# Kernel optimization log

Hardware: AMD Instinct MI355X
Metric: run time of the kernel (lower is better)

## Reference

```python
import jax, jax.numpy as jnp
import numpy as np

IN, MID, OUT = 512, 512, 512
B, S = 8, 1024
SLOPE = 0.01  # torch leaky_relu default


def _linear_params(key, fan_in, fan_out):
    # torch nn.Linear default init: U(-1/sqrt(fan_in), 1/sqrt(fan_in)) per real/imag part
    ks = jax.random.split(key, 4)
    bound = 1.0 / np.sqrt(fan_in)
    wr = jax.random.uniform(ks[0], (fan_out, fan_in), jnp.float32, -bound, bound)
    wi = jax.random.uniform(ks[1], (fan_out, fan_in), jnp.float32, -bound, bound)
    br = jax.random.uniform(ks[2], (fan_out,), jnp.float32, -bound, bound)
    bi = jax.random.uniform(ks[3], (fan_out,), jnp.float32, -bound, bound)
    return wr, wi, br, bi


def setup_inputs() -> dict:
    key = jax.random.key(0)
    ks = jax.random.split(key, 7)
    inp = {
        'x_real': jax.random.normal(ks[0], (B, S, IN), jnp.float32),
        'x_imag': jax.random.normal(ks[1], (B, S, IN), jnp.float32),
    }
    for name, k, fi, fo in [('l1', ks[2], IN, MID), ('q', ks[3], MID, MID),
                            ('k', ks[4], MID, MID), ('v', ks[5], MID, MID),
                            ('l2', ks[6], MID, OUT)]:
        wr, wi, br, bi = _linear_params(k, fi, fo)
        inp[f'{name}_wr'], inp[f'{name}_wi'] = wr, wi
        inp[f'{name}_br'], inp[f'{name}_bi'] = br, bi
    return inp


def _clin(x, wr, wi, br, bi):
    w = (wr + 1j * wi).astype(jnp.complex64)
    b = (br + 1j * bi).astype(jnp.complex64)
    return x @ w.T + b


def _lrelu_c(z):
    r = jnp.where(z.real >= 0, z.real, SLOPE * z.real)
    i = jnp.where(z.imag >= 0, z.imag, SLOPE * z.imag)
    return r + 1j * i


def reference(x_real, x_imag,
              l1_wr, l1_wi, l1_br, l1_bi,
              q_wr, q_wi, q_br, q_bi,
              k_wr, k_wi, k_br, k_bi,
              v_wr, v_wi, v_br, v_bi,
              l2_wr, l2_wi, l2_br, l2_bi):
    x = (x_real + 1j * x_imag).astype(jnp.complex64)
    y = _lrelu_c(_clin(x, l1_wr, l1_wi, l1_br, l1_bi))
    q = _clin(y, q_wr, q_wi, q_br, q_bi)
    k = _clin(y, k_wr, k_wi, k_br, k_bi)
    v = _clin(y, v_wr, v_wi, v_br, v_bi)
    scores = jnp.einsum('bsd,btd->bst', q, k) / jnp.sqrt(jnp.float32(MID))
    attn = jax.nn.softmax(jnp.abs(scores), axis=-1).astype(jnp.complex64)
    weighted = jnp.einsum('bst,btd->bsd', attn, v)
    out = _clin(weighted, l2_wr, l2_wi, l2_br, l2_bi)
    # return real/imag stacked as float32 for harness comparability
    return jnp.stack([out.real, out.imag], axis=0)
```

## Files before the change

### kernel.cpp

```cpp
#include <hip/hip_runtime.h>
#include <hip/hip_bf16.h>
#include <stdint.h>

typedef __hip_bfloat16 bf16;
typedef __attribute__((ext_vector_type(8))) short short8;
typedef __attribute__((ext_vector_type(4))) float f32x4;

#define DEVI __device__ __forceinline__

static constexpr long IMAG_OFF = 8192l * 512;

DEVI unsigned short f2b(float f) {
  bf16 h = __float2bfloat16(f);
  unsigned short u;
  __builtin_memcpy(&u, &h, 2);
  return u;
}

#define GLD16(g, l) __builtin_amdgcn_global_load_lds( \
    (const __attribute__((address_space(1))) void*)(g), \
    (__attribute__((address_space(3))) void*)(l), 16, 0, 0)

__global__ __launch_bounds__(256) void pack_x_kernel(
    const float* __restrict__ xr, const float* __restrict__ xi,
    unsigned short* __restrict__ xp) {
  const int t = blockIdx.x * 256 + threadIdx.x;
  const int m = t >> 8;
  const int d = (t & 255) * 4;
  const float* src = (d < 512) ? (xr + (long)m * 512 + d)
                               : (xi + (long)m * 512 + (d - 512));
  float4 v = *reinterpret_cast<const float4*>(src);
  ushort4 o;
  o.x = f2b(v.x); o.y = f2b(v.y); o.z = f2b(v.z); o.w = f2b(v.w);
  *reinterpret_cast<ushort4*>(xp + (long)m * 1024 + d) = o;
}

struct WArgs {
  const float* wr[5]; const float* wi[5];
  const float* br[5]; const float* bi[5];
};

__global__ __launch_bounds__(256) void pack_w_kernel(
    WArgs a, unsigned short* __restrict__ W, float* __restrict__ bias) {
  const int L = blockIdx.z;
  const int t = blockIdx.x * 256 + threadIdx.x;
  const int n = t >> 8;
  const int k = (t & 255) * 4;
  const float* wr = a.wr[L]; const float* wi = a.wi[L];
  const float* src; float sgn = 1.0f;
  if (n < 512) {
    if (k < 512) src = wr + (long)n * 512 + k;
    else { src = wi + (long)n * 512 + (k - 512); sgn = -1.0f; }
  } else {
    if (k < 512) src = wi + (long)(n - 512) * 512 + k;
    else         src = wr + (long)(n - 512) * 512 + (k - 512);
  }
  float4 v = *reinterpret_cast<const float4*>(src);
  ushort4 o;
  o.x = f2b(sgn * v.x); o.y = f2b(sgn * v.y);
  o.z = f2b(sgn * v.z); o.w = f2b(sgn * v.w);
  *reinterpret_cast<ushort4*>(W + (long)L * 1024 * 1024 + (long)n * 1024 + k) = o;
  if (t < 1024)
    bias[L * 1024 + t] = (t < 512) ? a.br[L][t] : a.bi[L][t - 512];
}

template<int OM, bool BIAS, bool ACT>
__global__ __launch_bounds__(512) void gemm3_kernel(
    const bf16* __restrict__ A, const bf16* __restrict__ Bm,
    void* __restrict__ C0, void* __restrict__ C1, void* __restrict__ C2,
    const float* __restrict__ bias, int N, int K, long sA, long sB, long sC) {
  __shared__ __align__(16) bf16 sm[3 * 12288];
  const int tid  = threadIdx.x;
  const int lane = tid & 63, wave = tid >> 6;
  const int r = lane & 15, g = lane >> 4;
  const int wr = wave >> 2, wc = wave & 3;
  const int m0 = blockIdx.x * 128, n0 = blockIdx.y * 256;
  const int z  = blockIdx.z;

  const bf16* Ab = A  + (long)z * sA;
  const bf16* Bb = Bm + (long)z * sB;
  const int srow = tid >> 2;
  const int schk = ((tid & 3) ^ ((tid >> 3) & 3)) * 8;
  const bf16* gA  = Ab + (long)(m0 + srow) * K + schk;
  const bf16* gB0 = Bb + (long)(n0 + srow) * K + schk;
  const bf16* gB1 = gB0 + (long)128 * K;
  char* const lb = (char*)sm + tid * 16;

#define STG3(buf, kt) do { \
    GLD16(gA  + (kt), lb + (buf) * 24576); \
    GLD16(gB0 + (kt), lb + (buf) * 24576 + 8192); \
    GLD16(gB1 + (kt), lb + (buf) * 24576 + 16384); } while (0)

  f32x4 acc[4][4] = {};
  const int sel = (g ^ ((r >> 1) & 3)) * 8;
  const int axoff = (wr * 64 + r) * 32 + sel;
  const int bxoff = 4096 + (wc * 64 + r) * 32 + sel;

  STG3(0, 0);
  STG3(1, 32);
  asm volatile("s_waitcnt vmcnt(3)" ::: "memory");
  __builtin_amdgcn_s_barrier();

  const int nt = K >> 5;
  int bc = 0, bs = 2;
  for (int t = 0; t < nt; ++t) {
    if (t + 2 < nt) STG3(bs, (t + 2) << 5);
    const bf16* S = sm + bc * 12288;
    short8 af[4], bq[4];
#pragma unroll
    for (int mi = 0; mi < 4; ++mi)
      af[mi] = *reinterpret_cast<const short8*>(S + axoff + mi * 512);
#pragma unroll
    for (int nj = 0; nj < 4; ++nj)
      bq[nj] = *reinterpret_cast<const short8*>(S + bxoff + nj * 512);
    __builtin_amdgcn_s_setprio(1);
#pragma unroll
    for (int mi = 0; mi < 4; ++mi)
#pragma unroll
      for (int nj = 0; nj < 4; ++nj)
        acc[mi][nj] = __builtin_amdgcn_mfma_f32_16x16x32_bf16(bq[nj], af[mi], acc[mi][nj], 0, 0, 0);
    __builtin_amdgcn_s_setprio(0);
    if (t < nt - 2) asm volatile("s_waitcnt vmcnt(3)" ::: "memory");
    else            asm volatile("s_waitcnt vmcnt(0)" ::: "memory");
    __builtin_amdgcn_s_barrier();
    bc = (bc == 2) ? 0 : bc + 1;
    bs = (bs == 2) ? 0 : bs + 1;
  }
#undef STG3

  const int rowbase = m0 + wr * 64 + r;
  const int colbase = n0 + wc * 64 + g * 4;
#pragma unroll
  for (int mi = 0; mi < 4; ++mi) {
    const long rm = rowbase + mi * 16;
#pragma unroll
    for (int nj = 0; nj < 4; ++nj) {
      const int cn = colbase + nj * 16;
      float4 f;
      f.x = acc[mi][nj][0]; f.y = acc[mi][nj][1];
      f.z = acc[mi][nj][2]; f.w = acc[mi][nj][3];
      if (BIAS) {
        float4 b4 = *reinterpret_cast<const float4*>(bias + cn);
        f.x += b4.x; f.y += b4.y; f.z += b4.z; f.w += b4.w;
      }
      if (ACT) {
        f.x = (f.x >= 0.f) ? f.x : 0.01f * f.x;
        f.y = (f.y >= 0.f) ? f.y : 0.01f * f.y;
        f.z = (f.z >= 0.f) ? f.z : 0.01f * f.z;
        f.w = (f.w >= 0.f) ? f.w : 0.01f * f.w;
      }
      if (OM == 0) {
        unsigned short* C = (unsigned short*)C0 + (long)z * sC;
        ushort4 o; o.x = f2b(f.x); o.y = f2b(f.y); o.z = f2b(f.z); o.w = f2b(f.w);
        *reinterpret_cast<ushort4*>(C + rm * N + cn) = o;
      } else if (OM == 2) {
        float* O = (float*)C0;
        if (cn < 512) *reinterpret_cast<float4*>(O + rm * 512 + cn) = f;
        else          *reinterpret_cast<float4*>(O + IMAG_OFF + rm * 512 + (cn - 512)) = f;
      } else if (OM == 3) {
        float* S = (float*)C0 + (long)z * sC;
        const float scale = 0.044194173824159216f;
        float2 mg;
        mg.x = sqrtf(f.x * f.x + f.y * f.y) * scale;
        mg.y = sqrtf(f.z * f.z + f.w * f.w) * scale;
        *reinterpret_cast<float2*>(S + rm * 1024 + (cn >> 1)) = mg;
      } else if (OM == 4) {
        if (cn < 1024) {
          unsigned short* Q = (unsigned short*)C0;
          ushort4 o; o.x = f2b(f.x); o.y = f2b(f.y); o.z = f2b(f.z); o.w = f2b(f.w);
          *reinterpret_cast<ushort4*>(Q + rm * 1024 + cn) = o;
        } else if (cn < 2048) {
          const int d = cn - 1024;
          const int b = (int)(rm >> 10), tt = (int)(rm & 1023);
          unsigned short* KM = (unsigned short*)C1;
          const float s = (d < 512) ? 1.0f : -1.0f;
          ushort4 o1, o2;
          o1.x = f2b(s * f.x); o1.y = f2b(s * f.y);
          o1.z = f2b(s * f.z); o1.w = f2b(s * f.w);
          o2.x = f2b(f.x); o2.y = f2b(f.y); o2.z = f2b(f.z); o2.w = f2b(f.w);
          *reinterpret_cast<ushort4*>(KM + ((long)(b << 11) + 2 * tt)     * 1024 + d)         = o1;
          *reinterpret_cast<ushort4*>(KM + ((long)(b << 11) + 2 * tt + 1) * 1024 + (d ^ 512)) = o2;
        } else {
          unsigned short* V = (unsigned short*)C2;
          ushort4 o; o.x = f2b(f.x); o.y = f2b(f.y); o.z = f2b(f.z); o.w = f2b(f.w);
          *reinterpret_cast<ushort4*>(V + rm * 1024 + (cn - 2048)) = o;
        }
      }
    }
  }
}

DEVI float wred_max(float v) {
#pragma unroll
  for (int o = 32; o > 0; o >>= 1) v = fmaxf(v, __shfl_xor(v, o));
  return v;
}
DEVI float wred_sum(float v) {
#pragma unroll
  for (int o = 32; o > 0; o >>= 1) v += __shfl_xor(v, o);
  return v;
}

__global__ __launch_bounds__(256) void softmax_kernel(
    const float* __restrict__ mag, unsigned short* __restrict__ attn) {
  const int row = blockIdx.x;
  const int tid = threadIdx.x;
  const int wave = tid >> 6, lane = tid & 63;
  float4 m4 = *reinterpret_cast<const float4*>(mag + (long)row * 1024 + tid * 4);
  float mx = fmaxf(fmaxf(m4.x, m4.y), fmaxf(m4.z, m4.w));
  mx = wred_max(mx);
  __shared__ float sred[8];
  if (lane == 0) sred[wave] = mx;
  __syncthreads();
  mx = fmaxf(fmaxf(sred[0], sred[1]), fmaxf(sred[2], sred[3]));
  float e[4];
  e[0] = expf(m4.x - mx); e[1] = expf(m4.y - mx);
  e[2] = expf(m4.z - mx); e[3] = expf(m4.w - mx);
  float s = e[0] + e[1] + e[2] + e[3];
  s = wred_sum(s);
  if (lane == 0) sred[4 + wave] = s;
  __syncthreads();
  s = sred[4] + sred[5] + sred[6] + sred[7];
  const float inv = 1.0f / s;
  ushort4 o;
  o.x = f2b(e[0] * inv); o.y = f2b(e[1] * inv);
  o.z = f2b(e[2] * inv); o.w = f2b(e[3] * inv);
  *reinterpret_cast<ushort4*>(attn + (long)row * 1024 + tid * 4) = o;
}

__global__ void transpose_kernel(const unsigned short* __restrict__ v,
                                 unsigned short* __restrict__ vt) {
  __shared__ unsigned short tile[32][33];
  const int b = blockIdx.z;
  const int t0 = blockIdx.x * 32, d0 = blockIdx.y * 32;
  const int tx = threadIdx.x, ty = threadIdx.y;
#pragma unroll
  for (int i = 0; i < 32; i += 8)
    tile[ty + i][tx] = v[((long)b * 1024 + t0 + ty + i) * 1024 + d0 + tx];
  __syncthreads();
#pragma unroll
  for (int i = 0; i < 32; i += 8)
    vt[((long)b * 1024 + d0 + ty + i) * 1024 + t0 + tx] = tile[tx][ty + i];
}

extern "C" void kernel_launch(void* const* d_in, const int* in_sizes, int n_in,
                              void* d_out, int out_size, void* d_ws, size_t ws_size,
                              hipStream_t stream) {
  const float* xr = (const float*)d_in[0];
  const float* xi = (const float*)d_in[1];
  WArgs wa;
  for (int L = 0; L < 5; ++L) {
    wa.wr[L] = (const float*)d_in[2 + 4 * L + 0];
    wa.wi[L] = (const float*)d_in[2 + 4 * L + 1];
    wa.br[L] = (const float*)d_in[2 + 4 * L + 2];
    wa.bi[L] = (const float*)d_in[2 + 4 * L + 3];
  }

  char* ws = (char*)d_ws;
  size_t off = 0;
  auto alloc = [&](size_t bytes) {
    char* p = ws + off;
    off += (bytes + 255) & ~(size_t)255;
    return p;
  };
  unsigned short* W    = (unsigned short*)alloc(5l * 1024 * 1024 * 2);
  float*          bias = (float*)         alloc(5l * 1024 * 4);
  unsigned short* xp   = (unsigned short*)alloc(8192l * 1024 * 2);
  unsigned short* y    = (unsigned short*)alloc(8192l * 1024 * 2);
  unsigned short* q    = (unsigned short*)alloc(8192l * 1024 * 2);
  unsigned short* kmod = (unsigned short*)alloc(8l * 2048 * 1024 * 2);
  unsigned short* v    = (unsigned short*)alloc(8192l * 1024 * 2);
  unsigned short* vt   = (unsigned short*)alloc(8l * 1024 * 1024 * 2);
  float*          mag  = (float*)         alloc(8l * 1024 * 1024 * 4);
  (void)ws_size; (void)in_sizes; (void)n_in; (void)out_size;

  pack_x_kernel<<<8192, 256, 0, stream>>>(xr, xi, xp);
  pack_w_kernel<<<dim3(1024, 1, 5), 256, 0, stream>>>(wa, W, bias);

  gemm3_kernel<0, true, true><<<dim3(64, 4, 1), 512, 0, stream>>>(
      (const bf16*)xp, (const bf16*)W, y, nullptr, nullptr, bias,
      1024, 1024, 0, 0, 0);

  gemm3_kernel<4, true, false><<<dim3(64, 12, 1), 512, 0, stream>>>(
      (const bf16*)y, (const bf16*)(W + 1l * 1024 * 1024), q, kmod, v,
      bias + 1024, 3072, 1024, 0, 0, 0);

  gemm3_kernel<3, false, false><<<dim3(8, 8, 8), 512, 0, stream>>>(
      (const bf16*)q, (const bf16*)kmod, mag, nullptr, nullptr, nullptr,
      2048, 1024, 1024l * 1024, 2048l * 1024, 1024l * 1024);

  softmax_kernel<<<8192, 256, 0, stream>>>(mag, xp );

  transpose_kernel<<<dim3(32, 32, 8), dim3(32, 8), 0, stream>>>(v, vt);

  gemm3_kernel<0, false, false><<<dim3(8, 4, 8), 512, 0, stream>>>(
      (const bf16*)xp, (const bf16*)vt, q , nullptr, nullptr,
      nullptr, 1024, 1024, 1024l * 1024, 1024l * 1024, 1024l * 1024);

  gemm3_kernel<2, true, false><<<dim3(64, 4, 1), 512, 0, stream>>>(
      (const bf16*)q, (const bf16*)(W + 4l * 1024 * 1024), d_out, nullptr,
      nullptr, bias + 4096, 1024, 1024, 0, 0, 0);
}
```

Measured before the change: 226.9 us.

## Add 256x256 ping-pong GEMM kernel for QKV and score GEMMs

Adds a new GEMM kernel with 256x256 output tiles, 128 KB double-buffered LDS staging and an eight-phase schedule that interleaves global-to-LDS loads with MFMA groups under barriers and raised wave priority. It is used for the fused QKV projection and the Q·K score magnitude GEMM. The QKV launch is also remapped to a swizzled 1D grid so neighbouring blocks share operand tiles in cache. The larger tiles cut redundant operand loads and aim to hide memory latency, at the cost of more registers and LDS per block, which leaves fewer resident blocks and fewer blocks for the batched score GEMM.

New measurement: 241.7 us. +6.5%, slower.

```diff
diff --git a/kernel.cpp b/kernel.cpp
--- a/kernel.cpp
+++ b/kernel.cpp
@@ -67,8 +67,8 @@
 template<int OM, bool BIAS, bool ACT>
 __global__ __launch_bounds__(512) void gemm3_kernel(
     const bf16* __restrict__ A, const bf16* __restrict__ Bm,
-    void* __restrict__ C0, void* __restrict__ C1, void* __restrict__ C2,
-    const float* __restrict__ bias, int N, int K, long sA, long sB, long sC) {
+    void* __restrict__ C0, const float* __restrict__ bias,
+    int N, int K, long sA, long sB, long sC) {
   __shared__ __align__(16) bf16 sm[3 * 12288];
   const int tid  = threadIdx.x;
   const int lane = tid & 63, wave = tid >> 6;
@@ -157,7 +157,157 @@
         float* O = (float*)C0;
         if (cn < 512) *reinterpret_cast<float4*>(O + rm * 512 + cn) = f;
         else          *reinterpret_cast<float4*>(O + IMAG_OFF + rm * 512 + (cn - 512)) = f;
-      } else if (OM == 3) {
+      }
+    }
+  }
+}
+
+template<int OM, bool BIAS>
+__global__ __launch_bounds__(512) void gemm8p_kernel(
+    const bf16* __restrict__ A, const bf16* __restrict__ Bm,
+    void* __restrict__ C0, void* __restrict__ C1, void* __restrict__ C2,
+    const float* __restrict__ bias,
+    int N, int K, long sA, long sB, long sC, int Mblocks, int Nblocks) {
+  __shared__ __align__(16) bf16 sm[65536];
+  const int tid  = threadIdx.x;
+  const int lane = tid & 63, wave = tid >> 6;
+  const int r = lane & 15, g = lane >> 4;
+  const int wr = wave >> 2, wc = wave & 3;
+
+  int bm, bn, z;
+  if (OM == 4) {
+    const int nn = blockIdx.x;
+    const int cpx = (Mblocks * Nblocks) >> 3;
+    const int swz = (nn & 7) * cpx + (nn >> 3);
+    bn = swz / Mblocks;
+    bm = swz - bn * Mblocks;
+    z = 0;
+  } else {
+    bm = blockIdx.x; bn = blockIdx.y; z = blockIdx.z;
+  }
+  const int m0 = bm * 256, n0 = bn * 256;
+
+  const bf16* Ab = A  + (long)z * sA;
+  const bf16* Bb = Bm + (long)z * sB;
+  const long K64 = (long)64 * K, K128 = (long)128 * K;
+  const int srow = tid >> 3;
+  const int schk = ((tid & 7) ^ (srow & 7)) * 8;
+  const bf16* gA    = Ab + (long)(m0 + srow) * K + schk;
+  const bf16* gA1   = gA + K128;
+  const bf16* gB    = Bb + (long)(n0 + srow) * K + schk;
+  const bf16* gB1   = gB + K128;
+  char* const lb = (char*)sm + tid * 16;
+
+  auto stg = [&](int buf, int half, const bf16* gp, long ko) {
+    char* d = lb + buf * 65536 + half * 16384;
+    GLD16(gp + ko, d);
+    GLD16(gp + ko + K64, d + 8192);
+  };
+
+  f32x4 acc[8][4] = {};
+  short8 fa[4][2], fb0[2][2], fb1[2][2];
+  const int arb = wr * 16 + r;
+  const int brb = wc * 16 + r;
+  int swze[2];
+  swze[0] = (g ^ (r & 7)) * 8;
+  swze[1] = ((g + 4) ^ (r & 7)) * 8;
+
+  auto rdA = [&](int buf, int half) {
+#pragma unroll
+    for (int m4 = 0; m4 < 4; ++m4) {
+      const bf16* rp = sm + buf * 32768 + half * 8192 + (m4 * 32 + arb) * 64;
+#pragma unroll
+      for (int kk = 0; kk < 2; ++kk)
+        fa[m4][kk] = *reinterpret_cast<const short8*>(rp + swze[kk]);
+    }
+  };
+  auto rdB = [&](int buf, int half, short8 (*fb)[2]) {
+#pragma unroll
+    for (int n2 = 0; n2 < 2; ++n2) {
+      const bf16* rp = sm + buf * 32768 + (2 + half) * 8192 + (n2 * 64 + brb) * 64;
+#pragma unroll
+      for (int kk = 0; kk < 2; ++kk)
+        fb[n2][kk] = *reinterpret_cast<const short8*>(rp + swze[kk]);
+    }
+  };
+
+#define MFMA16(MB, FB, NB) do { \
+    __builtin_amdgcn_s_setprio(1); \
+    _Pragma("unroll") \
+    for (int m4 = 0; m4 < 4; ++m4) \
+      _Pragma("unroll") \
+      for (int n2 = 0; n2 < 2; ++n2) \
+        _Pragma("unroll") \
+        for (int kk = 0; kk < 2; ++kk) \
+          acc[(MB) + m4][(NB) + n2] = __builtin_amdgcn_mfma_f32_16x16x32_bf16( \
+              FB[n2][kk], fa[m4][kk], acc[(MB) + m4][(NB) + n2], 0, 0, 0); \
+    __builtin_amdgcn_s_setprio(0); } while (0)
+
+#define PH_IN() do { \
+    asm volatile("" ::: "memory"); \
+    __builtin_amdgcn_s_barrier(); \
+    asm volatile("s_waitcnt lgkmcnt(0)" ::: "memory"); \
+    __builtin_amdgcn_sched_barrier(0); } while (0)
+#define VM(n) asm volatile("s_waitcnt vmcnt(" #n ")" ::: "memory")
+#define PH_OUT() __builtin_amdgcn_s_barrier()
+
+  stg(0, 0, gA, 0); stg(0, 2, gB, 0); stg(0, 3, gB1, 0); stg(0, 1, gA1, 0);
+  VM(0);
+  __builtin_amdgcn_s_barrier();
+
+  const int NT2 = K >> 7;
+  for (int t = 0; t < NT2; ++t) {
+    const long koO = (long)t * 128 + 64;
+    const long koE = (long)t * 128 + 128;
+    const bool more = (t + 1) < NT2;
+    rdA(0, 0); rdB(0, 0, fb0);
+    stg(1, 0, gA, koO);
+    PH_IN(); MFMA16(0, fb0, 0); VM(4); PH_OUT();
+    rdB(0, 1, fb1);
+    stg(1, 2, gB, koO);
+    PH_IN(); MFMA16(0, fb1, 2); VM(4); PH_OUT();
+    rdA(0, 1);
+    stg(1, 3, gB1, koO);
+    PH_IN(); MFMA16(4, fb1, 2); asm volatile("" ::: "memory"); PH_OUT();
+    stg(1, 1, gA1, koO);
+    PH_IN(); MFMA16(4, fb0, 0); VM(4); PH_OUT();
+    rdA(1, 0); rdB(1, 0, fb0);
+    if (more) stg(0, 0, gA, koE);
+    PH_IN(); MFMA16(0, fb0, 0);
+    if (more) { VM(4); } else { VM(2); }
+    PH_OUT();
+    rdB(1, 1, fb1);
+    if (more) stg(0, 2, gB, koE);
+    PH_IN(); MFMA16(0, fb1, 2);
+    if (more) { VM(4); } else { VM(0); }
+    PH_OUT();
+    rdA(1, 1);
+    if (more) stg(0, 3, gB1, koE);
+    PH_IN(); MFMA16(4, fb1, 2); asm volatile("" ::: "memory"); PH_OUT();
+    if (more) stg(0, 1, gA1, koE);
+    PH_IN(); MFMA16(4, fb0, 0);
+    if (more) { VM(4); } else { asm volatile("" ::: "memory"); }
+    PH_OUT();
+  }
+#undef MFMA16
+#undef PH_IN
+#undef PH_OUT
+#undef VM
+
+#pragma unroll
+  for (int mi = 0; mi < 8; ++mi) {
+    const long rm = m0 + (mi >> 2) * 128 + (mi & 3) * 32 + wr * 16 + r;
+#pragma unroll
+    for (int nj = 0; nj < 4; ++nj) {
+      const int cn = n0 + (nj >> 1) * 128 + (nj & 1) * 64 + wc * 16 + g * 4;
+      float4 f;
+      f.x = acc[mi][nj][0]; f.y = acc[mi][nj][1];
+      f.z = acc[mi][nj][2]; f.w = acc[mi][nj][3];
+      if (BIAS) {
+        float4 b4 = *reinterpret_cast<const float4*>(bias + cn);
+        f.x += b4.x; f.y += b4.y; f.z += b4.z; f.w += b4.w;
+      }
+      if (OM == 3) {
         float* S = (float*)C0 + (long)z * sC;
         const float scale = 0.044194173824159216f;
         float2 mg;
@@ -278,26 +428,25 @@
   pack_w_kernel<<<dim3(1024, 1, 5), 256, 0, stream>>>(wa, W, bias);
 
   gemm3_kernel<0, true, true><<<dim3(64, 4, 1), 512, 0, stream>>>(
-      (const bf16*)xp, (const bf16*)W, y, nullptr, nullptr, bias,
-      1024, 1024, 0, 0, 0);
-
-  gemm3_kernel<4, true, false><<<dim3(64, 12, 1), 512, 0, stream>>>(
+      (const bf16*)xp, (const bf16*)W, y, bias, 1024, 1024, 0, 0, 0);
+
+  gemm8p_kernel<4, true><<<dim3(384, 1, 1), 512, 0, stream>>>(
       (const bf16*)y, (const bf16*)(W + 1l * 1024 * 1024), q, kmod, v,
-      bias + 1024, 3072, 1024, 0, 0, 0);
-
-  gemm3_kernel<3, false, false><<<dim3(8, 8, 8), 512, 0, stream>>>(
+      bias + 1024, 3072, 1024, 0, 0, 0, 32, 12);
+
+  gemm8p_kernel<3, false><<<dim3(4, 8, 8), 512, 0, stream>>>(
       (const bf16*)q, (const bf16*)kmod, mag, nullptr, nullptr, nullptr,
-      2048, 1024, 1024l * 1024, 2048l * 1024, 1024l * 1024);
+      2048, 1024, 1024l * 1024, 2048l * 1024, 1024l * 1024, 4, 8);
 
   softmax_kernel<<<8192, 256, 0, stream>>>(mag, xp );
 
   transpose_kernel<<<dim3(32, 32, 8), dim3(32, 8), 0, stream>>>(v, vt);
 
   gemm3_kernel<0, false, false><<<dim3(8, 4, 8), 512, 0, stream>>>(
-      (const bf16*)xp, (const bf16*)vt, q , nullptr, nullptr,
-      nullptr, 1024, 1024, 1024l * 1024, 1024l * 1024, 1024l * 1024);
+      (const bf16*)xp, (const bf16*)vt, q , nullptr,
+      1024, 1024, 1024l * 1024, 1024l * 1024, 1024l * 1024);
 
   gemm3_kernel<2, true, false><<<dim3(64, 4, 1), 512, 0, stream>>>(
-      (const bf16*)q, (const bf16*)(W + 4l * 1024 * 1024), d_out, nullptr,
-      nullptr, bias + 4096, 1024, 1024, 0, 0, 0);
-}
+      (const bf16*)q, (const bf16*)(W + 4l * 1024 * 1024), d_out,
+      bias + 4096, 1024, 1024, 0, 0, 0);
+}
```

## Fuse V transpose into QKV GEMM epilogue and remap non-batched GEMM blocks for XCD locality

Applied to the files above, without the earlier changes.

The QKV projection epilogue now writes V directly in transposed layout (per-batch d-major), so the separate transpose kernel and the intermediate V buffer are removed. That saves one launch plus a full read and write of V. The non-batched GEMMs switch to a 1D grid whose block IDs are remapped so that consecutive tiles land on the same XCD chunk, to improve L2 reuse. The cost is that the transposed stores are scalar 2-byte writes strided by 1024 elements, which coalesce poorly compared with the old vectorized stores.

Result: no change. 224.6 us (-1.0%).

```diff
diff --git a/kernel.cpp b/kernel.cpp
--- a/kernel.cpp
+++ b/kernel.cpp
@@ -64,18 +64,30 @@
     bias[L * 1024 + t] = (t < 512) ? a.br[L][t] : a.bi[L][t - 512];
 }
 
-template<int OM, bool BIAS, bool ACT>
+template<int OM, bool BIAS, bool ACT, bool G1D>
 __global__ __launch_bounds__(512) void gemm3_kernel(
     const bf16* __restrict__ A, const bf16* __restrict__ Bm,
     void* __restrict__ C0, void* __restrict__ C1, void* __restrict__ C2,
-    const float* __restrict__ bias, int N, int K, long sA, long sB, long sC) {
+    const float* __restrict__ bias, int N, int K,
+    long sA, long sB, long sC, int Nb) {
   __shared__ __align__(16) bf16 sm[3 * 12288];
   const int tid  = threadIdx.x;
   const int lane = tid & 63, wave = tid >> 6;
   const int r = lane & 15, g = lane >> 4;
   const int wr = wave >> 2, wc = wave & 3;
-  const int m0 = blockIdx.x * 128, n0 = blockIdx.y * 256;
-  const int z  = blockIdx.z;
+
+  int bm, bn, z;
+  if (G1D) {
+    const int chunk = gridDim.x >> 3;
+    const int id = blockIdx.x;
+    const int c = (id & 7) * chunk + (id >> 3);
+    bm = c / Nb;
+    bn = c - bm * Nb;
+    z = 0;
+  } else {
+    bm = blockIdx.x; bn = blockIdx.y; z = blockIdx.z;
+  }
+  const int m0 = bm * 128, n0 = bn * 256;
 
   const bf16* Ab = A  + (long)z * sA;
   const bf16* Bb = Bm + (long)z * sB;
@@ -181,9 +193,14 @@
           *reinterpret_cast<ushort4*>(KM + ((long)(b << 11) + 2 * tt)     * 1024 + d)         = o1;
           *reinterpret_cast<ushort4*>(KM + ((long)(b << 11) + 2 * tt + 1) * 1024 + (d ^ 512)) = o2;
         } else {
-          unsigned short* V = (unsigned short*)C2;
-          ushort4 o; o.x = f2b(f.x); o.y = f2b(f.y); o.z = f2b(f.z); o.w = f2b(f.w);
-          *reinterpret_cast<ushort4*>(V + rm * 1024 + (cn - 2048)) = o;
+          unsigned short* VT = (unsigned short*)C2;
+          const int d = cn - 2048;
+          const int b = (int)(rm >> 10), tt = (int)(rm & 1023);
+          unsigned short* p = VT + ((long)b << 20) + (long)d * 1024 + tt;
+          p[0]    = f2b(f.x);
+          p[1024] = f2b(f.y);
+          p[2048] = f2b(f.z);
+          p[3072] = f2b(f.w);
         }
       }
     }
@@ -228,21 +245,6 @@
   *reinterpret_cast<ushort4*>(attn + (long)row * 1024 + tid * 4) = o;
 }
 
-__global__ void transpose_kernel(const unsigned short* __restrict__ v,
-                                 unsigned short* __restrict__ vt) {
-  __shared__ unsigned short tile[32][33];
-  const int b = blockIdx.z;
-  const int t0 = blockIdx.x * 32, d0 = blockIdx.y * 32;
-  const int tx = threadIdx.x, ty = threadIdx.y;
-#pragma unroll
-  for (int i = 0; i < 32; i += 8)
-    tile[ty + i][tx] = v[((long)b * 1024 + t0 + ty + i) * 1024 + d0 + tx];
-  __syncthreads();
-#pragma unroll
-  for (int i = 0; i < 32; i += 8)
-    vt[((long)b * 1024 + d0 + ty + i) * 1024 + t0 + tx] = tile[tx][ty + i];
-}
-
 extern "C" void kernel_launch(void* const* d_in, const int* in_sizes, int n_in,
                               void* d_out, int out_size, void* d_ws, size_t ws_size,
                               hipStream_t stream) {
@@ -269,7 +271,6 @@
   unsigned short* y    = (unsigned short*)alloc(8192l * 1024 * 2);
   unsigned short* q    = (unsigned short*)alloc(8192l * 1024 * 2);
   unsigned short* kmod = (unsigned short*)alloc(8l * 2048 * 1024 * 2);
-  unsigned short* v    = (unsigned short*)alloc(8192l * 1024 * 2);
   unsigned short* vt   = (unsigned short*)alloc(8l * 1024 * 1024 * 2);
   float*          mag  = (float*)         alloc(8l * 1024 * 1024 * 4);
   (void)ws_size; (void)in_sizes; (void)n_in; (void)out_size;
@@ -277,27 +278,25 @@
   pack_x_kernel<<<8192, 256, 0, stream>>>(xr, xi, xp);
   pack_w_kernel<<<dim3(1024, 1, 5), 256, 0, stream>>>(wa, W, bias);
 
-  gemm3_kernel<0, true, true><<<dim3(64, 4, 1), 512, 0, stream>>>(
+  gemm3_kernel<0, true, true, true><<<dim3(256, 1, 1), 512, 0, stream>>>(
       (const bf16*)xp, (const bf16*)W, y, nullptr, nullptr, bias,
-      1024, 1024, 0, 0, 0);
-
-  gemm3_kernel<4, true, false><<<dim3(64, 12, 1), 512, 0, stream>>>(
-      (const bf16*)y, (const bf16*)(W + 1l * 1024 * 1024), q, kmod, v,
-      bias + 1024, 3072, 1024, 0, 0, 0);
-
-  gemm3_kernel<3, false, false><<<dim3(8, 8, 8), 512, 0, stream>>>(
+      1024, 1024, 0, 0, 0, 4);
+
+  gemm3_kernel<4, true, false, true><<<dim3(768, 1, 1), 512, 0, stream>>>(
+      (const bf16*)y, (const bf16*)(W + 1l * 1024 * 1024), q, kmod, vt,
+      bias + 1024, 3072, 1024, 0, 0, 0, 12);
+
+  gemm3_kernel<3, false, false, false><<<dim3(8, 8, 8), 512, 0, stream>>>(
       (const bf16*)q, (const bf16*)kmod, mag, nullptr, nullptr, nullptr,
-      2048, 1024, 1024l * 1024, 2048l * 1024, 1024l * 1024);
+      2048, 1024, 1024l * 1024, 2048l * 1024, 1024l * 1024, 0);
 
   softmax_kernel<<<8192, 256, 0, stream>>>(mag, xp );
 
-  transpose_kernel<<<dim3(32, 32, 8), dim3(32, 8), 0, stream>>>(v, vt);
-
-  gemm3_kernel<0, false, false><<<dim3(8, 4, 8), 512, 0, stream>>>(
+  gemm3_kernel<0, false, false, false><<<dim3(8, 4, 8), 512, 0, stream>>>(
       (const bf16*)xp, (const bf16*)vt, q , nullptr, nullptr,
-      nullptr, 1024, 1024, 1024l * 1024, 1024l * 1024, 1024l * 1024);
-
-  gemm3_kernel<2, true, false><<<dim3(64, 4, 1), 512, 0, stream>>>(
+      nullptr, 1024, 1024, 1024l * 1024, 1024l * 1024, 1024l * 1024, 0);
+
+  gemm3_kernel<2, true, false, true><<<dim3(256, 1, 1), 512, 0, stream>>>(
       (const bf16*)q, (const bf16*)(W + 4l * 1024 * 1024), d_out, nullptr,
-      nullptr, bias + 4096, 1024, 1024, 0, 0, 0);
-}
+      nullptr, bias + 4096, 1024, 1024, 0, 0, 0, 4);
+}
```
